# Kernel optimization log

Hardware: AMD Instinct MI355X
Metric: run time of the kernel (lower is better)

Reference implementation:

```python
import jax, jax.numpy as jnp
import numpy as np

B, S, D, H, KV, HD = 2, 1024, 4096, 32, 8, 128
GROUP = H // KV


def setup_inputs() -> dict:
    key = jax.random.key(0)
    ks = jax.random.split(key, 9)
    x = jax.random.normal(ks[0], (B, S, D), dtype=jnp.float32)
    # RoPE tables: [max_seq_len, head_dim] (half-duplicated frequencies)
    pos = jnp.arange(S, dtype=jnp.float32)
    inv_freq = 1.0 / (10000.0 ** (jnp.arange(0, HD, 2, dtype=jnp.float32) / HD))
    freqs = pos[:, None] * inv_freq[None, :]            # [S, HD/2]
    emb = jnp.concatenate([freqs, freqs], axis=-1)      # [S, HD]
    cos, sin = jnp.cos(emb), jnp.sin(emb)
    # causal mask: True = masked
    mask = jnp.triu(jnp.ones((S, S), dtype=bool), 1)[None, None]  # [1,1,S,S]
    def qw(k, o, i):
        return jax.random.randint(k, (o, i), -127, 128, dtype=jnp.int8)
    wq = qw(ks[1], H * HD, D)
    wk = qw(ks[2], KV * HD, D)
    wv = qw(ks[3], KV * HD, D)
    wo = qw(ks[4], D, H * HD)
    sq = jnp.float32(0.02); sk = jnp.float32(0.02)
    sv = jnp.float32(0.02); so = jnp.float32(0.02)
    bq = jax.random.normal(ks[5], (H * HD,), jnp.float32) * 0.01
    bk = jax.random.normal(ks[6], (KV * HD,), jnp.float32) * 0.01
    bv = jax.random.normal(ks[7], (KV * HD,), jnp.float32) * 0.01
    return dict(x=x, mask=mask, cos=cos, sin=sin,
                wq=wq, bq=bq, sq=sq, wk=wk, bk=bk, sk=sk,
                wv=wv, bv=bv, sv=sv, wo=wo, so=so, start_pos=0)


def _deq_linear(x, w_int8, scale, bias):
    # dequantize-on-the-fly int8 linear: y = x @ (w.astype * scale).T + b
    w = w_int8.astype(x.dtype) * scale                  # [O, I]
    y = jnp.einsum('bsi,oi->bso', x, w)
    return y if bias is None else y + bias


def _rope(x, cos, sin, offset):
    # x: [b, s, h, hd]
    hd = x.shape[-1]
    x1, x2 = x[..., : hd // 2], x[..., hd // 2 :]
    s_len = x.shape[1]
    c = cos[offset : offset + s_len][None, :, None, :]
    s = sin[offset : offset + s_len][None, :, None, :]
    rotated = jnp.concatenate([-x2, x1], axis=-1)
    return (x * c + rotated * s).astype(x.dtype)


def reference(x, mask, cos, sin, wq, bq, sq, wk, bk, sk, wv, bv, sv, wo, so, start_pos):
    b, seq, _ = x.shape
    xq = _deq_linear(x, wq, sq, bq).reshape(b, seq, H, HD)
    xk = _deq_linear(x, wk, sk, bk).reshape(b, seq, KV, HD)
    xv = _deq_linear(x, wv, sv, bv).reshape(b, seq, KV, HD)
    xq = _rope(xq, cos, sin, start_pos)
    xk = _rope(xk, cos, sin, start_pos)
    # KV cache: start_pos=0 prefill -> cache[:start_pos+seq] == (xk, xv)
    kv_idx = jnp.arange(H) // GROUP                      # q head -> kv head
    keys = xk[:, :, kv_idx, :]                           # [b, kv_len, H, hd]
    values = xv[:, :, kv_idx, :]
    scores = jnp.einsum('bqhd,bkhd->bhqk', xq, keys) / np.sqrt(HD).astype(np.float32)
    scores = jnp.where(mask, -jnp.inf, scores)
    probs = jax.nn.softmax(scores, axis=-1)
    out = jnp.einsum('bhqk,bkhd->bqhd', probs, values).reshape(b, seq, H * HD)
    return _deq_linear(out, wo, so, None)
```

## Files before the change

### kernel.cpp

```cpp
#include <hip/hip_runtime.h>
#include <hip/hip_bf16.h>
#include <hip/hip_fp16.h>
#include <cstdint>

typedef _Float16 f16;
typedef _Float16 f16x8 __attribute__((ext_vector_type(8)));
typedef _Float16 f16x4 __attribute__((ext_vector_type(4)));
typedef float f32x4 __attribute__((ext_vector_type(4)));

#define DEV_INLINE __device__ __forceinline__

DEV_INLINE void async_ld16(const void* g, void* l) {
  __builtin_amdgcn_global_load_lds((const __attribute__((address_space(1))) void*)g,
                                   (__attribute__((address_space(3))) void*)l, 16, 0, 0);
}

template <int N>
DEV_INLINE void wait_vm() {
  static_assert(N >= 0 && N <= 12, "gate range");
  if constexpr (N == 0)  asm volatile("s_waitcnt vmcnt(0)" ::: "memory");
  if constexpr (N == 1)  asm volatile("s_waitcnt vmcnt(1)" ::: "memory");
  if constexpr (N == 2)  asm volatile("s_waitcnt vmcnt(2)" ::: "memory");
  if constexpr (N == 3)  asm volatile("s_waitcnt vmcnt(3)" ::: "memory");
  if constexpr (N == 4)  asm volatile("s_waitcnt vmcnt(4)" ::: "memory");
  if constexpr (N == 5)  asm volatile("s_waitcnt vmcnt(5)" ::: "memory");
  if constexpr (N == 6)  asm volatile("s_waitcnt vmcnt(6)" ::: "memory");
  if constexpr (N == 7)  asm volatile("s_waitcnt vmcnt(7)" ::: "memory");
  if constexpr (N == 8)  asm volatile("s_waitcnt vmcnt(8)" ::: "memory");
  if constexpr (N == 9)  asm volatile("s_waitcnt vmcnt(9)" ::: "memory");
  if constexpr (N == 10) asm volatile("s_waitcnt vmcnt(10)" ::: "memory");
  if constexpr (N == 11) asm volatile("s_waitcnt vmcnt(11)" ::: "memory");
  if constexpr (N == 12) asm volatile("s_waitcnt vmcnt(12)" ::: "memory");
}
DEV_INLINE void lgk0() {
  asm volatile("s_waitcnt lgkmcnt(0)" ::: "memory");
  __builtin_amdgcn_sched_barrier(0);
}

__global__ __launch_bounds__(256) void k_prep_all(
    const float* __restrict__ x,
    const int* __restrict__ wq, const int* __restrict__ wk, const int* __restrict__ wv,
    const float* __restrict__ bq, const float* __restrict__ bk, const float* __restrict__ bv,
    const float* __restrict__ sq, const float* __restrict__ sk, const float* __restrict__ sv,
    f16* __restrict__ acat, f16* __restrict__ wcat,
    float* __restrict__ bias_cat, float* __restrict__ scale_cat) {
  const int bid = blockIdx.x;
  if (bid < 8192) {
    int i = (bid * 256 + threadIdx.x) * 4;
    float4 v = *(const float4*)&x[i];
    int row = i >> 12, col = i & 4095;
    f16 h0 = (f16)v.x, h1 = (f16)v.y, h2 = (f16)v.z, h3 = (f16)v.w;
    f16x4 hi = {h0, h1, h2, h3};
    f16x4 lo = {(f16)(v.x - (float)h0), (f16)(v.y - (float)h1),
                (f16)(v.z - (float)h2), (f16)(v.w - (float)h3)};
    size_t base = (size_t)row * 8192 + col;
    *(f16x4*)&acat[base] = hi;
    *(f16x4*)&acat[base + 4096] = lo;
  } else {
    int i = (bid - 8192) * 256 + threadIdx.x;
    if (i < 6291456) {
      int e = i * 4, row = e >> 12, col = e & 4095;
      int4 v;
      if (row < 4096)      v = *(const int4*)&wq[(size_t)row * 4096 + col];
      else if (row < 5120) v = *(const int4*)&wk[(size_t)(row - 4096) * 4096 + col];
      else                 v = *(const int4*)&wv[(size_t)(row - 5120) * 4096 + col];
      f16x4 o = {(f16)(float)v.x, (f16)(float)v.y, (f16)(float)v.z, (f16)(float)v.w};
      *(f16x4*)&wcat[e] = o;
    }
    if (i < 6144) {
      float b, s;
      if (i < 4096)      { b = bq[i];        s = sq[0]; }
      else if (i < 5120) { b = bk[i - 4096]; s = sk[0]; }
      else               { b = bv[i - 5120]; s = sv[0]; }
      bias_cat[i] = b;
      scale_cat[i] = s;
    }
  }
}

__global__ __launch_bounds__(256) void k_cast_i32_f16(const int* __restrict__ w,
                                                      f16* __restrict__ out, int n) {
  int i = (blockIdx.x * 256 + threadIdx.x) * 4;
  if (i >= n) return;
  int4 v = *(const int4*)&w[i];
  f16x4 o = {(f16)(float)v.x, (f16)(float)v.y, (f16)(float)v.z, (f16)(float)v.w};
  *(f16x4*)&out[i] = o;
}

template <int BM, int BN, int MODE>
__global__ __launch_bounds__(512) void k_gemm6(
    const f16* __restrict__ A, const f16* __restrict__ W,
    f16* __restrict__ o_hi, f16* __restrict__ o_lo, float* __restrict__ o_f32,
    const float* __restrict__ scale_vec, const float* __restrict__ bias_vec,
    const float* __restrict__ scale_scalar,
    int N, int K, int kmask, int ldw, int nym) {
  constexpr int WM = 2, WN = 4;
  constexpr int MR = BM / WM / 16;
  constexpr int NR = BN / WN / 16;
  constexpr int NH = NR / 2;
  constexpr int AKC = BM * 64;
  constexpr int BKC = BN * 64;
  constexpr int SLOT = 2 * (AKC + BKC);
  constexpr int LAH = AKC / 8192;
  constexpr int LBH = BKC / 8192;
  constexpr int GS = 2 * LBH + 3;
  constexpr int GT1 = 2 * LBH + 2;
  constexpr int GT2 = LBH + 1;
  extern __shared__ __align__(16) char lds[];

  const int t = threadIdx.x, w = t >> 6, ln = t & 63;
  const int lr = ln & 15, lg = ln >> 4;
  const int wn = w & 3, wm = w >> 2;

  const int nwg = gridDim.x;
  const int q8 = nwg >> 3, r8 = nwg & 7;
  const int xcd = blockIdx.x & 7, bidx = blockIdx.x >> 3;
  const int sid = (xcd < r8 ? xcd * (q8 + 1) : r8 * (q8 + 1) + (xcd - r8) * q8) + bidx;
  const int m0 = (sid % nym) * BM;
  const int n0 = (sid / nym) * BN;

  const f16* aSrc[LAH];
  const f16* bSrc[LBH];
#pragma unroll
  for (int l = 0; l < LAH; l++) {
    int ci = l * 512 + t, row = ci >> 2, c = ci & 3;
    aSrc[l] = A + (size_t)(m0 + row) * K + (c ^ ((row >> 1) & 3)) * 8;
  }
#pragma unroll
  for (int l = 0; l < LBH; l++) {
    int ci = l * 512 + t, row = ci >> 2, c = ci & 3;
    bSrc[l] = W + (size_t)(n0 + row) * ldw + (c ^ ((row >> 1) & 3)) * 8;
  }

  f32x4 acc[MR][NR] = {};
  f16x8 af[MR], bflo[NH], bfhi[NH];

  auto stageA = [&](int tt, int kc) {
    char* dst = lds + (tt & 1) * SLOT + kc * AKC;
    const int ko = tt * 64 + kc * 32;
#pragma unroll
    for (int l = 0; l < LAH; l++)
      async_ld16(aSrc[l] + ko, dst + (l * 512 + w * 64) * 16);
  };
  auto stageB = [&](int tt, int kc) {
    char* dst = lds + (tt & 1) * SLOT + 2 * AKC + kc * BKC;
    const int ko = ((tt * 64) & kmask) + kc * 32;
#pragma unroll
    for (int l = 0; l < LBH; l++)
      async_ld16(bSrc[l] + ko, dst + (l * 512 + w * 64) * 16);
  };
  auto readA = [&](int tt, int kc) {
    const char* base = lds + (tt & 1) * SLOT + kc * AKC;
#pragma unroll
    for (int mf = 0; mf < MR; mf++) {
      const int row = wm * (BM / WM) + mf * 16 + lr;
      af[mf] = *(const f16x8*)(base + row * 64 + (lg ^ ((row >> 1) & 3)) * 16);
    }
  };
  auto readB = [&](f16x8 (&dst)[NH], int tt, int nq, int kc) {
    const char* base = lds + (tt & 1) * SLOT + 2 * AKC + kc * BKC;
#pragma unroll
    for (int nf = 0; nf < NH; nf++) {
      const int row = wn * (BN / WN) + (nq * NH + nf) * 16 + lr;
      dst[nf] = *(const f16x8*)(base + row * 64 + (lg ^ ((row >> 1) & 3)) * 16);
    }
  };
  auto mma = [&](f16x8 (&b)[NH], int nq) {
    __builtin_amdgcn_s_setprio(1);
#pragma unroll
    for (int m = 0; m < MR; m++)
#pragma unroll
      for (int n = 0; n < NH; n++)
        acc[m][nq * NH + n] =
            __builtin_amdgcn_mfma_f32_16x16x32_f16(af[m], b[n], acc[m][nq * NH + n], 0, 0, 0);
    __builtin_amdgcn_s_setprio(0);
  };
  auto bar = [&]() { __builtin_amdgcn_s_barrier(); };

  const int NT = K >> 6;
  stageA(0, 0); stageB(0, 0); stageA(0, 1); stageB(0, 1);
  stageA(1, 0); stageB(1, 0); stageA(1, 1);
  wait_vm<GS>();
  bar();

  for (int tt = 0; tt + 2 < NT; ++tt) {
    stageB(tt + 1, 1);
    readA(tt, 0); readB(bflo, tt, 0, 0);
    bar(); lgk0(); mma(bflo, 0); bar();
    stageA(tt + 2, 0);
    readB(bfhi, tt, 1, 0);
    wait_vm<GS>();
    bar(); lgk0(); mma(bfhi, 1); bar();
    stageB(tt + 2, 0);
    readA(tt, 1); readB(bflo, tt, 0, 1);
    bar(); lgk0(); mma(bflo, 0); bar();
    stageA(tt + 2, 1);
    readB(bfhi, tt, 1, 1);
    wait_vm<GS>();
    bar(); lgk0(); mma(bfhi, 1); bar();
  }
  {
    const int tt = NT - 2;
    stageB(tt + 1, 1);
    readA(tt, 0); readB(bflo, tt, 0, 0);
    bar(); lgk0(); mma(bflo, 0); bar();
    readB(bfhi, tt, 1, 0);
    wait_vm<GT1>();
    bar(); lgk0(); mma(bfhi, 1); bar();
    readA(tt, 1); readB(bflo, tt, 0, 1);
    bar(); lgk0(); mma(bflo, 0); bar();
    readB(bfhi, tt, 1, 1);
    wait_vm<GT2>();
    bar(); lgk0(); mma(bfhi, 1); bar();
  }
  {
    const int tt = NT - 1;
    readA(tt, 0); readB(bflo, tt, 0, 0);
    bar(); lgk0(); mma(bflo, 0); bar();
    readB(bfhi, tt, 1, 0);
    wait_vm<0>();
    bar(); lgk0(); mma(bfhi, 1); bar();
    readA(tt, 1); readB(bflo, tt, 0, 1);
    bar(); lgk0(); mma(bflo, 0); bar();
    readB(bfhi, tt, 1, 1);
    bar(); lgk0(); mma(bfhi, 1);
  }

#pragma unroll
  for (int n = 0; n < NR; n++) {
    const int col = n0 + wn * (BN / WN) + n * 16 + lr;
    const float sc = (MODE == 0) ? scale_vec[col] : scale_scalar[0];
    const float bs = (MODE == 0) ? bias_vec[col] : 0.f;
#pragma unroll
    for (int m = 0; m < MR; m++)
#pragma unroll
      for (int r2 = 0; r2 < 4; r2++) {
        const int row = m0 + wm * (BM / WM) + m * 16 + lg * 4 + r2;
        const float v = acc[m][n][r2] * sc + bs;
        if constexpr (MODE == 0) {
          f16 h = (f16)v;
          o_hi[(size_t)row * N + col] = h;
          o_lo[(size_t)row * N + col] = (f16)(v - (float)h);
        } else {
          o_f32[(size_t)row * N + col] = v;
        }
      }
  }
}

__global__ __launch_bounds__(256) void k_rope2(f16* __restrict__ XH, f16* __restrict__ XL,
                                               const float* __restrict__ cosT,
                                               const float* __restrict__ sinT,
                                               const int* __restrict__ sp) {
  int idx = blockIdx.x * 256 + threadIdx.x;
  if (idx >= 2048 * 40 * 16) return;
  int c4 = (idx & 15) * 4;
  int hh = (idx >> 4) % 40;
  int tkn = idx / (40 * 16);
  int col = (hh < 32) ? hh * 128 : 4096 + (hh - 32) * 128;
  size_t i1 = (size_t)tkn * 6144 + col + c4, i2 = i1 + 64;
  int pos = (tkn & 1023) + sp[0];
  const float4 cv = *(const float4*)&cosT[pos * 128 + c4];
  const float4 sv = *(const float4*)&sinT[pos * 128 + c4];
  f16x4 xh1 = *(const f16x4*)&XH[i1], xh2 = *(const f16x4*)&XH[i2];
  f16x4 xl1 = *(const f16x4*)&XL[i1], xl2 = *(const f16x4*)&XL[i2];
  f16x4 oh1, ol1, oh2, ol2;
  const float cc[4] = {cv.x, cv.y, cv.z, cv.w};
  const float ss[4] = {sv.x, sv.y, sv.z, sv.w};
#pragma unroll
  for (int i = 0; i < 4; i++) {
    float x1 = (float)xh1[i] + (float)xl1[i];
    float x2 = (float)xh2[i] + (float)xl2[i];
    float o1 = x1 * cc[i] - x2 * ss[i];
    float o2 = x2 * cc[i] + x1 * ss[i];
    f16 h1 = (f16)o1, h2 = (f16)o2;
    oh1[i] = h1; ol1[i] = (f16)(o1 - (float)h1);
    oh2[i] = h2; ol2[i] = (f16)(o2 - (float)h2);
  }
  *(f16x4*)&XH[i1] = oh1; *(f16x4*)&XL[i1] = ol1;
  *(f16x4*)&XH[i2] = oh2; *(f16x4*)&XL[i2] = ol2;
}

__global__ __launch_bounds__(512) void k_attn4(const f16* __restrict__ XH,
                                               const f16* __restrict__ XL,
                                               f16* __restrict__ out) {
  __shared__ __align__(16) f16 KsH[32 * 152];
  __shared__ __align__(16) f16 KsL[32 * 152];
  __shared__ __align__(16) f16 VT[128 * 40];
  __shared__ __align__(16) f16 Pb[8 * 16 * 40];
  const int t = threadIdx.x, w = t >> 6, l = t & 63;
  const int lr = l & 15, lg = l >> 4;
  const int id = blockIdx.x;
  const int kvh = id & 7;
  const int j = id >> 3;
  const int qb = j & 7;
  const int hg = (j >> 3) & 3;
  const int b = j >> 5;
  const int h = kvh * 4 + hg;
  const int q0 = qb * 128;
  const size_t rs_ = 6144;
  const f16* Qh = XH + ((size_t)(b * 1024 + q0)) * rs_ + h * 128;
  const f16* Ql_ = XL + ((size_t)(b * 1024 + q0)) * rs_ + h * 128;
  const f16* KhG = XH + ((size_t)(b * 1024)) * rs_ + 4096 + kvh * 128;
  const f16* KlG = XL + ((size_t)(b * 1024)) * rs_ + 4096 + kvh * 128;
  const f16* VG = XH + ((size_t)(b * 1024)) * rs_ + 5120 + kvh * 128;

  f16x8 qh[4], ql[4];
  {
    size_t qoff = (size_t)(w * 16 + lr) * rs_ + lg * 8;
#pragma unroll
    for (int c = 0; c < 4; c++) {
      qh[c] = *(const f16x8*)(Qh + qoff + c * 32);
      ql[c] = *(const f16x8*)(Ql_ + qoff + c * 32);
    }
  }
  f32x4 accd[8] = {};
  float m_r[4], l_r[4];
#pragma unroll
  for (int r = 0; r < 4; r++) { m_r[r] = -1e30f; l_r[r] = 0.f; }

  const int krow_s = t >> 4, kch = t & 15;
  const int vrow_s = t & 31, vd8 = t >> 5;
  f16x8 khr, klr, vr;
  auto loadKV = [&](int kv0) {
    size_t go = (size_t)(kv0 + krow_s) * rs_ + kch * 8;
    khr = *(const f16x8*)(KhG + go);
    klr = *(const f16x8*)(KlG + go);
    vr = *(const f16x8*)(VG + (size_t)(kv0 + vrow_s) * rs_ + vd8 * 8);
  };
  auto writeKV = [&]() {
    *(f16x8*)&KsH[krow_s * 152 + kch * 8] = khr;
    *(f16x8*)&KsL[krow_s * 152 + kch * 8] = klr;
#pragma unroll
    for (int jj = 0; jj < 8; jj++) VT[(vd8 * 8 + jj) * 40 + vrow_s] = vr[jj];
  };

  const int nkv = q0 + 128;
  const int NT = nkv >> 5;
  loadKV(0);
  wait_vm<0>();
  writeKV();
  __syncthreads();

  for (int tt = 0; tt < NT; ++tt) {
    const int kv0 = tt * 32;
    const bool pf = (tt + 1 < NT);
    if (pf) {
      loadKV(kv0 + 32);
      __builtin_amdgcn_sched_barrier(0);
    }

    f32x4 sc[2] = {};
#pragma unroll
    for (int cb = 0; cb < 2; cb++)
#pragma unroll
      for (int c = 0; c < 4; c++) {
        const f16x8 kh = *(const f16x8*)&KsH[(cb * 16 + lr) * 152 + c * 32 + lg * 8];
        const f16x8 kl = *(const f16x8*)&KsL[(cb * 16 + lr) * 152 + c * 32 + lg * 8];
        sc[cb] = __builtin_amdgcn_mfma_f32_16x16x32_f16(qh[c], kh, sc[cb], 0, 0, 0);
        sc[cb] = __builtin_amdgcn_mfma_f32_16x16x32_f16(qh[c], kl, sc[cb], 0, 0, 0);
        sc[cb] = __builtin_amdgcn_mfma_f32_16x16x32_f16(ql[c], kh, sc[cb], 0, 0, 0);
      }

    const float scale = 0.088388347648318447f;
    float alpha[4], pv[2][4];
#pragma unroll
    for (int r = 0; r < 4; r++) {
      const int qg = q0 + w * 16 + lg * 4 + r;
      float mx = -1e30f;
#pragma unroll
      for (int cb = 0; cb < 2; cb++) {
        const int kg = kv0 + cb * 16 + lr;
        float s = sc[cb][r] * scale;
        s = (kg <= qg) ? s : -1e30f;
        pv[cb][r] = s;
        mx = fmaxf(mx, s);
      }
      mx = fmaxf(mx, __shfl_xor(mx, 1));
      mx = fmaxf(mx, __shfl_xor(mx, 2));
      mx = fmaxf(mx, __shfl_xor(mx, 4));
      mx = fmaxf(mx, __shfl_xor(mx, 8));
      const float mn = fmaxf(m_r[r], mx);
      alpha[r] = __expf(m_r[r] - mn);
      m_r[r] = mn;
      float rsum = 0.f;
#pragma unroll
      for (int cb = 0; cb < 2; cb++) {
        const int kg = kv0 + cb * 16 + lr;
        const float p = (kg <= qg) ? __expf(pv[cb][r] - mn) : 0.f;
        pv[cb][r] = p;
        rsum += p;
      }
      rsum += __shfl_xor(rsum, 1);
      rsum += __shfl_xor(rsum, 2);
      rsum += __shfl_xor(rsum, 4);
      rsum += __shfl_xor(rsum, 8);
      l_r[r] = l_r[r] * alpha[r] + rsum;
    }

    f16* Pw = &Pb[w * 16 * 40];
#pragma unroll
    for (int r = 0; r < 4; r++)
#pragma unroll
      for (int cb = 0; cb < 2; cb++)
        Pw[(lg * 4 + r) * 40 + cb * 16 + lr] = (f16)pv[cb][r];
    const f16x8 pf_ = *(const f16x8*)&Pw[lr * 40 + lg * 8];

#pragma unroll
    for (int dc = 0; dc < 8; dc++) {
      const f16x8 vf = *(const f16x8*)&VT[(dc * 16 + lr) * 40 + lg * 8];
#pragma unroll
      for (int r = 0; r < 4; r++) accd[dc][r] *= alpha[r];
      accd[dc] = __builtin_amdgcn_mfma_f32_16x16x32_f16(pf_, vf, accd[dc], 0, 0, 0);
    }

    __syncthreads();
    if (pf) writeKV();
    __syncthreads();
  }

#pragma unroll
  for (int dc = 0; dc < 8; dc++)
#pragma unroll
    for (int r = 0; r < 4; r++) {
      const int row = b * 1024 + q0 + w * 16 + lg * 4 + r;
      out[(size_t)row * 4096 + h * 128 + dc * 16 + lr] = (f16)(accd[dc][r] / l_r[r]);
    }
}

extern "C" void kernel_launch(void* const* d_in, const int* in_sizes, int n_in,
                              void* d_out, int out_size, void* d_ws, size_t ws_size,
                              hipStream_t stream) {
  const float* x = (const float*)d_in[0];
  const float* cosT = (const float*)d_in[2];
  const float* sinT = (const float*)d_in[3];
  const int* wq = (const int*)d_in[4];
  const float* bq = (const float*)d_in[5];
  const float* sq = (const float*)d_in[6];
  const int* wk = (const int*)d_in[7];
  const float* bk = (const float*)d_in[8];
  const float* sk = (const float*)d_in[9];
  const int* wv = (const int*)d_in[10];
  const float* bv = (const float*)d_in[11];
  const float* sv = (const float*)d_in[12];
  const int* wo = (const int*)d_in[13];
  const float* so = (const float*)d_in[14];
  const int* sp = (const int*)d_in[15];

  char* ws = (char*)d_ws;
  f16* Acat = (f16*)ws;
  f16* Wcat = (f16*)(ws + 33554432);
  f16* XH = (f16*)(ws + 83886080);
  f16* XL = (f16*)(ws + 109051904);
  f16* AO = (f16*)(ws + 134217728);
  float* biasv = (float*)(ws + 150994944);
  float* scalev = (float*)(ws + 151019520);

  hipFuncSetAttribute(reinterpret_cast<const void*>(&k_gemm6<128, 384, 0>),
                      hipFuncAttributeMaxDynamicSharedMemorySize, 131072);
  hipFuncSetAttribute(reinterpret_cast<const void*>(&k_gemm6<128, 256, 1>),
                      hipFuncAttributeMaxDynamicSharedMemorySize, 98304);

  k_prep_all<<<32768, 256, 0, stream>>>(x, wq, wk, wv, bq, bk, bv, sq, sk, sv,
                                        Acat, Wcat, biasv, scalev);

  k_gemm6<128, 384, 0><<<256, 512, 131072, stream>>>(
      Acat, Wcat, XH, XL, nullptr, scalev, biasv, nullptr, 6144, 8192, 4095, 4096, 16);

  k_rope2<<<5120, 256, 0, stream>>>(XH, XL, cosT, sinT, sp);

  f16* Wo_ = Acat;
  k_cast_i32_f16<<<16384, 256, 0, stream>>>(wo, Wo_, 16777216);

  k_attn4<<<512, 512, 0, stream>>>(XH, XL, AO);

  k_gemm6<128, 256, 1><<<256, 512, 98304, stream>>>(
      AO, Wo_, nullptr, nullptr, (float*)d_out, nullptr, nullptr, so, 4096, 4096,
      0x7fffffff, 4096, 16);
}
```

Baseline: 479.9 us.

## Restructure GEMM pipeline to full-B fragment reads with two MMA phases per tile

The GEMM main loop moves from four half-width MFMA phases per K tile, each guarded by its own barriers and staggered async loads, to two phases that read all B fragments at once and issue the full MR×NR MFMA block. Async staging is regrouped so A and B chunks for a k-half are issued together, and the vmcnt gates are recomputed. The goal is to halve barrier and wait overhead per tile and give each phase larger MFMA bursts. In exchange it raises register pressure from holding all B fragments and shortens the prefetch lookahead, which can expose more global-load latency.

```diff
diff --git a/kernel.cpp b/kernel.cpp
--- a/kernel.cpp
+++ b/kernel.cpp
@@ -88,7 +88,7 @@
 }
 
 template <int BM, int BN, int MODE>
-__global__ __launch_bounds__(512) void k_gemm6(
+__global__ __launch_bounds__(512) void k_gemm8(
     const f16* __restrict__ A, const f16* __restrict__ W,
     f16* __restrict__ o_hi, f16* __restrict__ o_lo, float* __restrict__ o_f32,
     const float* __restrict__ scale_vec, const float* __restrict__ bias_vec,
@@ -97,15 +97,13 @@
   constexpr int WM = 2, WN = 4;
   constexpr int MR = BM / WM / 16;
   constexpr int NR = BN / WN / 16;
-  constexpr int NH = NR / 2;
   constexpr int AKC = BM * 64;
   constexpr int BKC = BN * 64;
   constexpr int SLOT = 2 * (AKC + BKC);
   constexpr int LAH = AKC / 8192;
   constexpr int LBH = BKC / 8192;
-  constexpr int GS = 2 * LBH + 3;
-  constexpr int GT1 = 2 * LBH + 2;
-  constexpr int GT2 = LBH + 1;
+  constexpr int GS = 2 * (LAH + LBH);
+  constexpr int G1 = LAH + LBH;
   extern __shared__ __align__(16) char lds[];
 
   const int t = threadIdx.x, w = t >> 6, ln = t & 63;
@@ -133,7 +131,7 @@
   }
 
   f32x4 acc[MR][NR] = {};
-  f16x8 af[MR], bflo[NH], bfhi[NH];
+  f16x8 af[MR], bfa[NR];
 
   auto stageA = [&](int tt, int kc) {
     char* dst = lds + (tt & 1) * SLOT + kc * AKC;
@@ -157,73 +155,58 @@
       af[mf] = *(const f16x8*)(base + row * 64 + (lg ^ ((row >> 1) & 3)) * 16);
     }
   };
-  auto readB = [&](f16x8 (&dst)[NH], int tt, int nq, int kc) {
+  auto readBall = [&](int tt, int kc) {
     const char* base = lds + (tt & 1) * SLOT + 2 * AKC + kc * BKC;
 #pragma unroll
-    for (int nf = 0; nf < NH; nf++) {
-      const int row = wn * (BN / WN) + (nq * NH + nf) * 16 + lr;
-      dst[nf] = *(const f16x8*)(base + row * 64 + (lg ^ ((row >> 1) & 3)) * 16);
-    }
-  };
-  auto mma = [&](f16x8 (&b)[NH], int nq) {
+    for (int nf = 0; nf < NR; nf++) {
+      const int row = wn * (BN / WN) + nf * 16 + lr;
+      bfa[nf] = *(const f16x8*)(base + row * 64 + (lg ^ ((row >> 1) & 3)) * 16);
+    }
+  };
+  auto mma = [&]() {
     __builtin_amdgcn_s_setprio(1);
 #pragma unroll
     for (int m = 0; m < MR; m++)
 #pragma unroll
-      for (int n = 0; n < NH; n++)
-        acc[m][nq * NH + n] =
-            __builtin_amdgcn_mfma_f32_16x16x32_f16(af[m], b[n], acc[m][nq * NH + n], 0, 0, 0);
+      for (int n = 0; n < NR; n++)
+        acc[m][n] = __builtin_amdgcn_mfma_f32_16x16x32_f16(af[m], bfa[n], acc[m][n], 0, 0, 0);
     __builtin_amdgcn_s_setprio(0);
   };
   auto bar = [&]() { __builtin_amdgcn_s_barrier(); };
 
   const int NT = K >> 6;
   stageA(0, 0); stageB(0, 0); stageA(0, 1); stageB(0, 1);
-  stageA(1, 0); stageB(1, 0); stageA(1, 1);
+  stageA(1, 0); stageB(1, 0);
   wait_vm<GS>();
   bar();
 
   for (int tt = 0; tt + 2 < NT; ++tt) {
-    stageB(tt + 1, 1);
-    readA(tt, 0); readB(bflo, tt, 0, 0);
-    bar(); lgk0(); mma(bflo, 0); bar();
-    stageA(tt + 2, 0);
-    readB(bfhi, tt, 1, 0);
+    stageA(tt + 1, 1); stageB(tt + 1, 1);
+    readA(tt, 0); readBall(tt, 0);
     wait_vm<GS>();
-    bar(); lgk0(); mma(bfhi, 1); bar();
-    stageB(tt + 2, 0);
-    readA(tt, 1); readB(bflo, tt, 0, 1);
-    bar(); lgk0(); mma(bflo, 0); bar();
-    stageA(tt + 2, 1);
-    readB(bfhi, tt, 1, 1);
+    bar(); lgk0(); mma(); bar();
+    stageA(tt + 2, 0); stageB(tt + 2, 0);
+    readA(tt, 1); readBall(tt, 1);
     wait_vm<GS>();
-    bar(); lgk0(); mma(bfhi, 1); bar();
+    bar(); lgk0(); mma(); bar();
   }
   {
     const int tt = NT - 2;
-    stageB(tt + 1, 1);
-    readA(tt, 0); readB(bflo, tt, 0, 0);
-    bar(); lgk0(); mma(bflo, 0); bar();
-    readB(bfhi, tt, 1, 0);
-    wait_vm<GT1>();
-    bar(); lgk0(); mma(bfhi, 1); bar();
-    readA(tt, 1); readB(bflo, tt, 0, 1);
-    bar(); lgk0(); mma(bflo, 0); bar();
-    readB(bfhi, tt, 1, 1);
-    wait_vm<GT2>();
-    bar(); lgk0(); mma(bfhi, 1); bar();
+    stageA(tt + 1, 1); stageB(tt + 1, 1);
+    readA(tt, 0); readBall(tt, 0);
+    wait_vm<GS>();
+    bar(); lgk0(); mma(); bar();
+    readA(tt, 1); readBall(tt, 1);
+    wait_vm<G1>();
+    bar(); lgk0(); mma(); bar();
   }
   {
     const int tt = NT - 1;
-    readA(tt, 0); readB(bflo, tt, 0, 0);
-    bar(); lgk0(); mma(bflo, 0); bar();
-    readB(bfhi, tt, 1, 0);
+    readA(tt, 0); readBall(tt, 0);
     wait_vm<0>();
-    bar(); lgk0(); mma(bfhi, 1); bar();
-    readA(tt, 1); readB(bflo, tt, 0, 1);
-    bar(); lgk0(); mma(bflo, 0); bar();
-    readB(bfhi, tt, 1, 1);
-    bar(); lgk0(); mma(bfhi, 1);
+    bar(); lgk0(); mma(); bar();
+    readA(tt, 1); readBall(tt, 1);
+    lgk0(); mma();
   }
 
 #pragma unroll
@@ -456,15 +439,15 @@
   float* biasv = (float*)(ws + 150994944);
   float* scalev = (float*)(ws + 151019520);
 
-  hipFuncSetAttribute(reinterpret_cast<const void*>(&k_gemm6<128, 384, 0>),
+  hipFuncSetAttribute(reinterpret_cast<const void*>(&k_gemm8<128, 384, 0>),
                       hipFuncAttributeMaxDynamicSharedMemorySize, 131072);
-  hipFuncSetAttribute(reinterpret_cast<const void*>(&k_gemm6<128, 256, 1>),
+  hipFuncSetAttribute(reinterpret_cast<const void*>(&k_gemm8<128, 256, 1>),
                       hipFuncAttributeMaxDynamicSharedMemorySize, 98304);
 
   k_prep_all<<<32768, 256, 0, stream>>>(x, wq, wk, wv, bq, bk, bv, sq, sk, sv,
                                         Acat, Wcat, biasv, scalev);
 
-  k_gemm6<128, 384, 0><<<256, 512, 131072, stream>>>(
+  k_gemm8<128, 384, 0><<<256, 512, 131072, stream>>>(
       Acat, Wcat, XH, XL, nullptr, scalev, biasv, nullptr, 6144, 8192, 4095, 4096, 16);
 
   k_rope2<<<5120, 256, 0, stream>>>(XH, XL, cosT, sinT, sp);
@@ -474,7 +457,7 @@
 
   k_attn4<<<512, 512, 0, stream>>>(XH, XL, AO);
 
-  k_gemm6<128, 256, 1><<<256, 512, 98304, stream>>>(
+  k_gemm8<128, 256, 1><<<256, 512, 98304, stream>>>(
       AO, Wo_, nullptr, nullptr, (float*)d_out, nullptr, nullptr, so, 4096, 4096,
       0x7fffffff, 4096, 16);
 }
```

New measurement: 481.2 us. About the same (+0.3%).
